# Kernel tuning notes

Measured on AMD Instinct MI355X. Metric: run time of the kernel, lower is better.

Reference implementation:

```python
import jax, jax.numpy as jnp
from jax import lax
import numpy as np

B, H, W = 8, 1024, 1024
NUM_POINTS = 10
THRESHOLD_RATIO = 0.5
K_PEAKS = 512  # cap on peak candidates fed to greedy NMS


def setup_inputs() -> dict:
    key = jax.random.key(0)
    ks = jax.random.split(key, 8)
    return {
        "rgb_image": jax.random.uniform(ks[0], (B, 3, H, W), jnp.float32),
        "depth_image": jax.random.uniform(ks[1], (B, 1, H, W), jnp.float32),
        "conv1_w": jax.random.normal(ks[2], (32, 12, 3, 3), jnp.float32) * 0.1,
        "conv1_b": jax.random.normal(ks[3], (32,), jnp.float32) * 0.1,
        "bn_gamma": jnp.ones((32,), jnp.float32),
        "bn_beta": jnp.zeros((32,), jnp.float32),
        "bn_mean": jax.random.normal(ks[4], (32,), jnp.float32) * 0.1,
        "bn_var": jax.random.uniform(ks[5], (32,), jnp.float32) + 0.5,
        "conv2_w": jax.random.normal(ks[6], (1, 32, 1, 1), jnp.float32) * 0.1,
        "conv2_b": jnp.zeros((1,), jnp.float32),
    }


def dwt2(x):
    # Haar DWT exactly as in the torch module (row split then column split)
    x01 = x[..., 0::2, :] * 0.5
    x02 = x[..., 1::2, :] * 0.5
    LL = x01[..., 0::2] + x02[..., 0::2]
    LH = x01[..., 0::2] - x02[..., 0::2]
    HL = x01[..., 1::2] + x02[..., 1::2]
    HH = x01[..., 1::2] - x02[..., 1::2]
    return LL, LH, HL, HH


def conv2d(x, w, b=None, pad=0, groups=1):
    y = lax.conv_general_dilated(x, w, (1, 1), [(pad, pad), (pad, pad)],
                                 dimension_numbers=("NCHW", "OIHW", "NCHW"),
                                 feature_group_count=groups)
    if b is not None:
        y = y + b[None, :, None, None]
    return y


def gaussian_smooth(x, k=5, sigma=1.0):
    ax = jnp.arange(-(k // 2), k // 2 + 1, dtype=jnp.float32)
    xx, yy = jnp.meshgrid(ax, ax, indexing="ij")
    ker = jnp.exp(-(xx ** 2 + yy ** 2) / (2.0 * sigma ** 2))
    ker = ker / ker.sum()
    C = x.shape[1]
    wk = jnp.tile(ker[None, None], (C, 1, 1, 1))  # depthwise
    return conv2d(x, wk, pad=k // 2, groups=C)


def find_points(s):
    """Greedy spatial-NMS peak picking on a single (h,w) saliency map.
    Returns (NUM_POINTS, 2) normalized (x, y) coords."""
    h, w = s.shape
    min_dist = float(max(max(h, w) // 20, 20))
    flat = s.reshape(-1)
    mp = lax.reduce_window(s, -jnp.inf, lax.max, (3, 3), (1, 1), [(1, 1), (1, 1)])
    peak_flat = ((s == mp) & (s > 0)).reshape(-1)
    peak_scores = jnp.where(peak_flat, flat, -jnp.inf)
    top_vals, top_idx = lax.top_k(peak_scores, K_PEAKS)  # sorted desc = torch argsort
    valid = top_vals > -jnp.inf
    px = (top_idx % w).astype(jnp.float32)
    py = (top_idx // w).astype(jnp.float32)
    pc = jnp.stack([px, py], axis=-1)                     # (K,2)
    dist = jnp.sqrt(((pc[:, None, :] - pc[None, :, :]) ** 2).sum(-1))  # (K,K)
    ar = jnp.arange(K_PEAKS)

    def body(i, st):
        avail, sel, cnt = st
        take = avail[i] & valid[i] & (cnt < NUM_POINTS)
        sel = sel.at[i].set(take)
        suppress = (dist[i] < min_dist) & (ar > i)  # nearby[:i+1]=False in torch
        avail = jnp.where(take, avail & (~suppress), avail)
        return avail, sel, cnt + take.astype(jnp.int32)

    _, sel, n_chosen = lax.fori_loop(
        0, K_PEAKS, body,
        (jnp.ones(K_PEAKS, bool), jnp.zeros(K_PEAKS, bool), jnp.int32(0)))

    # compact chosen peak indices (in descending-score order) into first slots
    pos = jnp.cumsum(sel.astype(jnp.int32)) - 1
    scatter_pos = jnp.where(sel, pos, NUM_POINTS)  # out-of-range -> dropped
    buf = jnp.zeros(NUM_POINTS, jnp.int32).at[scatter_pos].set(top_idx, mode="drop")
    # fallback: top saliency excluding all peaks (matches torch fill-up branch)
    fb_scores = jnp.where(peak_flat, -jnp.inf, flat)
    _, fb_idx = lax.top_k(fb_scores, NUM_POINTS)
    slot = jnp.arange(NUM_POINTS)
    fb = fb_idx[jnp.clip(slot - n_chosen, 0, NUM_POINTS - 1)]
    sel_idx = jnp.where(slot < n_chosen, buf, fb)
    cx = (sel_idx % w).astype(jnp.float32) / w
    cy = (sel_idx // w).astype(jnp.float32) / h
    return jnp.stack([cx, cy], axis=-1)


def boxes_from_mask(masks):
    binm = masks[:, 0] > THRESHOLD_RATIO  # (B,H,W)
    Hh, Ww = binm.shape[1], binm.shape[2]
    rows = binm.any(axis=2)
    cols = binm.any(axis=1)
    ri = jnp.arange(Hh)
    ci = jnp.arange(Ww)
    rmin = jnp.min(jnp.where(rows, ri[None, :], Hh), axis=1)
    rmax = jnp.max(jnp.where(rows, ri[None, :], -1), axis=1)
    cmin = jnp.min(jnp.where(cols, ci[None, :], Ww), axis=1)
    cmax = jnp.max(jnp.where(cols, ci[None, :], -1), axis=1)
    has = rows.any(axis=1)
    boxes = jnp.stack([cmin, rmin, cmax, rmax], axis=-1).astype(jnp.float32)
    default = jnp.array([0.0, 0.0, Ww - 1.0, Hh - 1.0], jnp.float32)
    return jnp.where(has[:, None], boxes, default[None, :])


def reference(rgb_image, depth_image, conv1_w, conv1_b, bn_gamma, bn_beta,
              bn_mean, bn_var, conv2_w, conv2_b):
    rgb_gray = rgb_image.mean(axis=1, keepdims=True)
    rLL, rLH, rHL, rHH = dwt2(rgb_gray)
    dLL, dLH, dHL, dHH = dwt2(depth_image)
    E_rgb = jnp.sqrt(rLH ** 2 + rHL ** 2 + rHH ** 2 + 1e-8)
    E_depth = jnp.sqrt(dLH ** 2 + dHL ** 2 + dHH ** 2 + 1e-8)
    E_rgb_s = gaussian_smooth(E_rgb)
    E_depth_s = gaussian_smooth(E_depth)
    freq = jnp.concatenate(
        [rLL, rLH, rHL, rHH, dLL, dLH, dHL, dHH, E_rgb, E_depth, E_rgb_s, E_depth_s],
        axis=1)  # (B,12,H/2,W/2)
    x = conv2d(freq, conv1_w, conv1_b, pad=1)
    inv = lax.rsqrt(bn_var + 1e-5)
    x = bn_gamma[None, :, None, None] * (x - bn_mean[None, :, None, None]) * inv[None, :, None, None] + bn_beta[None, :, None, None]
    x = jax.nn.gelu(x)
    sal = jax.nn.sigmoid(conv2d(x, conv2_w, conv2_b))  # (B,1,H/2,W/2)
    masks = jax.image.resize(sal, (sal.shape[0], 1, H, W), method="bilinear")
    coords = jax.vmap(find_points)(sal[:, 0])          # (B,N,2)
    labels = jnp.ones((sal.shape[0], NUM_POINTS), jnp.int32)
    boxes = boxes_from_mask(masks)                     # (B,4)
    return coords, labels, boxes, masks
```

## Files before the change

kernel.cpp:

```cpp
#include <hip/hip_runtime.h>
#include <math.h>


#define CHW 262144
#define FULLHW 1048576
#define NB1 64
#define NB2 32

typedef __attribute__((ext_vector_type(8))) short bf16x8;
typedef __attribute__((ext_vector_type(4))) float f32x4;

static __device__ __forceinline__ unsigned short f2bf(float x) {
  unsigned u = __float_as_uint(x);
  u += 0x7FFFu + ((u >> 16) & 1u);
  return (unsigned short)(u >> 16);
}
static __device__ __forceinline__ float bf2f(unsigned short h) {
  return __uint_as_float(((unsigned)h) << 16);
}

static constexpr size_t OFF_SAL   = 0;
static constexpr size_t OFF_THR   = 8388608;
static constexpr size_t OFF_CNT   = OFF_THR + 256;
static constexpr size_t OFF_CAND  = OFF_CNT + 256;
static constexpr size_t OFF_PART  = OFF_CAND + 131072;
static constexpr size_t OFF_APACK = OFF_PART + 32768;
static constexpr size_t OFF_EP    = OFF_APACK + 20480;
static constexpr size_t OFF_PKM   = OFF_EP + 512;
static constexpr size_t OFF_DYN   = OFF_PKM + 2097152;

static constexpr int KDY[10] = {-1,-1,-1, 0,0,0, 1,1,1, 0};
static constexpr int KDX[10] = {-1, 0, 1,-1,0,1,-1,0,1, 0};

__global__ void k_init(unsigned* __restrict__ cnt,
                       const float* __restrict__ w1, const float* __restrict__ b1,
                       const float* __restrict__ gam, const float* __restrict__ bet,
                       const float* __restrict__ mean, const float* __restrict__ var,
                       const float* __restrict__ w2, const float* __restrict__ b2,
                       unsigned short* __restrict__ apack, float* __restrict__ ep) {
  int i = blockIdx.x * 256 + threadIdx.x;
  if (i < 16) cnt[i] = 0;
  if (i < 10240) {
    int frag = i >> 9, lane = (i >> 3) & 63, e = i & 7;
    int hh = frag & 1, mtks = frag >> 1;
    int mt = mtks / 5, ks = mtks % 5;
    int co = mt * 16 + (lane & 15);
    int k = ((lane >> 4) << 3) + e;
    int c = k & 15, shift = ks * 2 + (k >> 4);
    float val = (shift < 9 && c < 12) ? w1[co * 108 + c * 9 + shift] : 0.0f;
    unsigned short hb = f2bf(val);
    apack[i] = hh ? f2bf(val - bf2f(hb)) : hb;
  }
  int j = i - 10240;
  if (j >= 0 && j < 97) {
    if (j < 32) {
      ep[j] = gam[j] * rsqrtf(var[j] + 1e-5f);
    } else if (j < 64) {
      int c = j - 32;
      float sc = gam[c] * rsqrtf(var[c] + 1e-5f);
      ep[j] = (b1[c] - mean[c]) * sc + bet[c];
    } else if (j < 96) {
      ep[j] = w2[j - 64];
    } else {
      ep[j] = b2[0];
    }
  }
}

__global__ __launch_bounds__(256) void k_freq(const float* __restrict__ rgb,
                                              const float* __restrict__ dep,
                                              unsigned short* __restrict__ freq2,
                                              float* __restrict__ ebuf, int b0) {
  int t = blockIdx.x * 256 + threadIdx.x;
  int bi = blockIdx.y;
  int b = b0 + bi;
  int xp = t & 255, y = t >> 8;
  const float* base = rgb + (size_t)b * 3 * FULLHW + (size_t)(2 * y) * 1024 + 4 * xp;
  float4 R0 = *(const float4*)(base);
  float4 R1 = *(const float4*)(base + 1024);
  float4 G0 = *(const float4*)(base + FULLHW);
  float4 G1 = *(const float4*)(base + FULLHW + 1024);
  float4 Bl0 = *(const float4*)(base + 2 * FULLHW);
  float4 Bl1 = *(const float4*)(base + 2 * FULLHW + 1024);
  const float* dbase = dep + (size_t)b * FULLHW + (size_t)(2 * y) * 1024 + 4 * xp;
  float4 D0 = *(const float4*)(dbase);
  float4 D1 = *(const float4*)(dbase + 1024);

  float gt[4], gb[4], dt[4], db_[4];
  gt[0] = (R0.x + G0.x + Bl0.x) / 3.0f; gt[1] = (R0.y + G0.y + Bl0.y) / 3.0f;
  gt[2] = (R0.z + G0.z + Bl0.z) / 3.0f; gt[3] = (R0.w + G0.w + Bl0.w) / 3.0f;
  gb[0] = (R1.x + G1.x + Bl1.x) / 3.0f; gb[1] = (R1.y + G1.y + Bl1.y) / 3.0f;
  gb[2] = (R1.z + G1.z + Bl1.z) / 3.0f; gb[3] = (R1.w + G1.w + Bl1.w) / 3.0f;
  dt[0] = D0.x; dt[1] = D0.y; dt[2] = D0.z; dt[3] = D0.w;
  db_[0] = D1.x; db_[1] = D1.y; db_[2] = D1.z; db_[3] = D1.w;

  unsigned short hs[2][16], ls[2][16];
  float er[2], ed[2];
  #pragma unroll
  for (int j = 0; j < 2; ++j) {
    float a = gt[2 * j] * 0.5f, bb = gb[2 * j] * 0.5f;
    float c = gt[2 * j + 1] * 0.5f, d = gb[2 * j + 1] * 0.5f;
    float v[10];
    v[0] = a + bb; v[1] = a - bb; v[2] = c + d; v[3] = c - d;
    float da = dt[2 * j] * 0.5f, db2 = db_[2 * j] * 0.5f;
    float dc = dt[2 * j + 1] * 0.5f, dd = db_[2 * j + 1] * 0.5f;
    v[4] = da + db2; v[5] = da - db2; v[6] = dc + dd; v[7] = dc - dd;
    v[8] = sqrtf(v[1] * v[1] + v[2] * v[2] + v[3] * v[3] + 1e-8f);
    v[9] = sqrtf(v[5] * v[5] + v[6] * v[6] + v[7] * v[7] + 1e-8f);
    er[j] = v[8]; ed[j] = v[9];
    #pragma unroll
    for (int cc = 0; cc < 10; ++cc) {
      unsigned short hb = f2bf(v[cc]);
      hs[j][cc] = hb;
      ls[j][cc] = f2bf(v[cc] - bf2f(hb));
    }
    #pragma unroll
    for (int cc = 10; cc < 16; ++cc) { hs[j][cc] = 0; ls[j][cc] = 0; }
  }
  unsigned short* dst = freq2 + (size_t)bi * CHW * 32 + (size_t)(y * 512 + 2 * xp) * 32;
  uint4* d4 = (uint4*)dst;
  d4[0] = ((const uint4*)hs[0])[0]; d4[1] = ((const uint4*)hs[0])[1];
  d4[2] = ((const uint4*)ls[0])[0]; d4[3] = ((const uint4*)ls[0])[1];
  d4[4] = ((const uint4*)hs[1])[0]; d4[5] = ((const uint4*)hs[1])[1];
  d4[6] = ((const uint4*)ls[1])[0]; d4[7] = ((const uint4*)ls[1])[1];
  float* eb = ebuf + (size_t)bi * 2 * CHW + (size_t)y * 512 + 2 * xp;
  *(float2*)(eb) = make_float2(er[0], er[1]);
  *(float2*)(eb + CHW) = make_float2(ed[0], ed[1]);
}

__constant__ float GW[25] = {
  0.00296901f, 0.01330621f, 0.02193824f, 0.01330621f, 0.00296901f,
  0.01330621f, 0.05963435f, 0.09832035f, 0.05963435f, 0.01330621f,
  0.02193824f, 0.09832035f, 0.16210276f, 0.09832035f, 0.02193824f,
  0.01330621f, 0.05963435f, 0.09832035f, 0.05963435f, 0.01330621f,
  0.00296901f, 0.01330621f, 0.02193824f, 0.01330621f, 0.00296901f};

__global__ __launch_bounds__(256) void k_smooth(const float* __restrict__ ebuf,
                                                unsigned short* __restrict__ freq2) {
  int t = blockIdx.x * 256 + threadIdx.x;
  int bi = blockIdx.y;
  int x = t & 511, y = t >> 9;
  const float* eb = ebuf + (size_t)bi * 2 * CHW;
  float accv[2];
  #pragma unroll
  for (int ch = 0; ch < 2; ++ch) {
    const float* fin = eb + ch * CHW;
    float acc = 0.0f;
    #pragma unroll
    for (int i = 0; i < 5; ++i) {
      int yy = y + i - 2;
      if (yy < 0 || yy > 511) continue;
      #pragma unroll
      for (int j = 0; j < 5; ++j) {
        int xx = x + j - 2;
        if (xx < 0 || xx > 511) continue;
        acc += GW[i * 5 + j] * fin[yy * 512 + xx];
      }
    }
    accv[ch] = acc;
  }
  unsigned short* px = freq2 + (size_t)bi * CHW * 32 + (size_t)t * 32;
  unsigned short h0 = f2bf(accv[0]), h1 = f2bf(accv[1]);
  unsigned short l0 = f2bf(accv[0] - bf2f(h0)), l1 = f2bf(accv[1] - bf2f(h1));
  *(unsigned*)(px + 10) = (unsigned)h0 | ((unsigned)h1 << 16);
  *(unsigned*)(px + 26) = (unsigned)l0 | ((unsigned)l1 << 16);
}

__global__ __launch_bounds__(256) void k_conv(const unsigned short* __restrict__ freq2,
    const unsigned short* __restrict__ apack, const float* __restrict__ ep,
    float* __restrict__ sal, int b0) {
  int tid = threadIdx.x;
  int l = tid & 63, wv = tid >> 6;
  int y = blockIdx.y;
  int xw = blockIdx.x * 128 + wv * 32;
  int bi = blockIdx.z;
  const unsigned short* fb = freq2 + (size_t)bi * CHW * 32;

  int ln = l & 15, lg = l >> 4;
  int sl = lg >> 1;
  int c0 = (lg & 1) << 3;

  float sc[8], sh[8], w2v[8];
  #pragma unroll
  for (int mt = 0; mt < 2; ++mt)
    #pragma unroll
    for (int r = 0; r < 4; ++r) {
      int co = mt * 16 + lg * 4 + r;
      sc[mt * 4 + r]  = ep[co];
      sh[mt * 4 + r]  = ep[32 + co];
      w2v[mt * 4 + r] = ep[64 + co];
    }
  float b2v = ep[96];

  f32x4 acc[2][2] = {};

  #pragma unroll
  for (int ks = 0; ks < 5; ++ks) {
    int dy = sl ? KDY[ks * 2 + 1] : KDY[ks * 2];
    int dx = sl ? KDX[ks * 2 + 1] : KDX[ks * 2];
    int yy = y + dy;
    bool yok = (unsigned)yy < 512u;
    bf16x8 Ah[2], Al[2];
    #pragma unroll
    for (int mt = 0; mt < 2; ++mt) {
      const unsigned short* ab = apack + ((size_t)((mt * 5 + ks) * 2) * 64 + l) * 8;
      Ah[mt] = *(const bf16x8*)(ab);
      Al[mt] = *(const bf16x8*)(ab + 512);
    }
    #pragma unroll
    for (int nt = 0; nt < 2; ++nt) {
      int xx = xw + nt * 16 + ln + dx;
      bf16x8 Bh = {}, Bl = {};
      if (yok && (unsigned)xx < 512u) {
        const unsigned short* pb = fb + (size_t)(yy * 512 + xx) * 32 + c0;
        Bh = *(const bf16x8*)(pb);
        Bl = *(const bf16x8*)(pb + 16);
      }
      #pragma unroll
      for (int mt = 0; mt < 2; ++mt) {
        acc[mt][nt] = __builtin_amdgcn_mfma_f32_16x16x32_bf16(Ah[mt], Bh, acc[mt][nt], 0, 0, 0);
        acc[mt][nt] = __builtin_amdgcn_mfma_f32_16x16x32_bf16(Al[mt], Bh, acc[mt][nt], 0, 0, 0);
        acc[mt][nt] = __builtin_amdgcn_mfma_f32_16x16x32_bf16(Ah[mt], Bl, acc[mt][nt], 0, 0, 0);
      }
    }
  }

  #pragma unroll
  for (int nt = 0; nt < 2; ++nt) {
    float s2 = 0.0f;
    #pragma unroll
    for (int mt = 0; mt < 2; ++mt)
      #pragma unroll
      for (int r = 0; r < 4; ++r) {
        float t = acc[mt][nt][r] * sc[mt * 4 + r] + sh[mt * 4 + r];
        float t2 = t * t;
        float z = t * (1.5957691216057308f + 0.07135481283247183f * t2);
        float g = t / (1.0f + __expf(-z));
        s2 += g * w2v[mt * 4 + r];
      }
    s2 += __shfl_xor(s2, 16);
    s2 += __shfl_xor(s2, 32);
    s2 += b2v;
    float res = 1.0f / (1.0f + __expf(-s2));
    if (lg == 0)
      sal[(size_t)(b0 + bi) * CHW + (size_t)y * 512 + xw + nt * 16 + ln] = res;
  }
}

__global__ __launch_bounds__(256) void k_resize(const float* __restrict__ sal,
                                                float* __restrict__ masks,
                                                int* __restrict__ part) {
  int b = blockIdx.y;
  int blk = blockIdx.x;
  int t = threadIdx.x;
  const float* sp = sal + (size_t)b * CHW;
  float* mp = masks + (size_t)b * FULLHW;
  int mnX = 0x7FFFFFFF, mxX = -1, mnY = 0x7FFFFFFF, mxY = -1;
  int c0 = 4 * t;
  #pragma unroll
  for (int r = 0; r < 4; ++r) {
    int Y = blk * 4 + r;
    int y0 = (Y - 1) >> 1;
    float wy = (Y & 1) ? 0.25f : 0.75f;
    int y0c = y0 < 0 ? 0 : y0, y1c = (y0 + 1 > 511) ? 511 : y0 + 1;
    const float* r0 = sp + y0c * 512;
    const float* r1 = sp + y1c * 512;
    float o[4];
    #pragma unroll
    for (int j = 0; j < 4; ++j) {
      int X = c0 + j;
      int x0 = (X - 1) >> 1;
      float wx = (X & 1) ? 0.25f : 0.75f;
      int x0c = x0 < 0 ? 0 : x0, x1c = (x0 + 1 > 511) ? 511 : x0 + 1;
      float v00 = r0[x0c], v01 = r0[x1c], v10 = r1[x0c], v11 = r1[x1c];
      o[j] = (1.0f - wy) * ((1.0f - wx) * v00 + wx * v01)
           + wy * ((1.0f - wx) * v10 + wx * v11);
      if (o[j] > 0.5f) {
        mnX = min(mnX, X); mxX = max(mxX, X);
        mnY = min(mnY, Y); mxY = max(mxY, Y);
      }
    }
    *(float4*)(mp + (size_t)Y * 1024 + c0) = make_float4(o[0], o[1], o[2], o[3]);
  }
  __shared__ int s0[256], s1[256], s2[256], s3[256];
  s0[t] = mnX; s1[t] = mxX; s2[t] = mnY; s3[t] = mxY;
  __syncthreads();
  for (int off = 128; off > 0; off >>= 1) {
    if (t < off) {
      s0[t] = min(s0[t], s0[t + off]); s1[t] = max(s1[t], s1[t + off]);
      s2[t] = min(s2[t], s2[t + off]); s3[t] = max(s3[t], s3[t + off]);
    }
    __syncthreads();
  }
  if (t == 0) {
    int* pp = part + (b * 256 + blk) * 4;
    pp[0] = s0[0]; pp[1] = s1[0]; pp[2] = s2[0]; pp[3] = s3[0];
  }
}

__global__ __launch_bounds__(256) void k_boxreduce(const int* __restrict__ part,
                                                   float* __restrict__ out) {
  int b = blockIdx.x, t = threadIdx.x;
  const int* pp = part + (b * 256 + t) * 4;
  __shared__ int s0[256], s1[256], s2[256], s3[256];
  s0[t] = pp[0]; s1[t] = pp[1]; s2[t] = pp[2]; s3[t] = pp[3];
  __syncthreads();
  for (int off = 128; off > 0; off >>= 1) {
    if (t < off) {
      s0[t] = min(s0[t], s0[t + off]); s1[t] = max(s1[t], s1[t + off]);
      s2[t] = min(s2[t], s2[t + off]); s3[t] = max(s3[t], s3[t + off]);
    }
    __syncthreads();
  }
  if (t == 0) {
    float x0, y0, x1, y1;
    if (s3[0] < 0) { x0 = 0.0f; y0 = 0.0f; x1 = 1023.0f; y1 = 1023.0f; }
    else { x0 = (float)s0[0]; y0 = (float)s2[0]; x1 = (float)s1[0]; y1 = (float)s3[0]; }
    out[240 + b * 4 + 0] = x0;
    out[240 + b * 4 + 1] = y0;
    out[240 + b * 4 + 2] = x1;
    out[240 + b * 4 + 3] = y1;
  }
}

__device__ inline bool is_peak(const float* __restrict__ sp, int x, int y, float& sv) {
  float s = sp[y * 512 + x];
  sv = s;
  if (!(s > 0.0f)) return false;
  int x0 = (x > 0) ? x - 1 : x, x1 = (x < 511) ? x + 1 : x;
  int y0 = (y > 0) ? y - 1 : y, y1 = (y < 511) ? y + 1 : y;
  for (int yy = y0; yy <= y1; ++yy)
    for (int xx = x0; xx <= x1; ++xx)
      if (sp[yy * 512 + xx] > s) return false;
  return true;
}

__global__ __launch_bounds__(256) void k_hist1(const float* __restrict__ sal,
                                               unsigned* __restrict__ h1p,
                                               unsigned char* __restrict__ pkm) {
  __shared__ unsigned sH[4096];
  int b = blockIdx.y, tid = threadIdx.x;
  for (int i = tid; i < 4096; i += 256) sH[i] = 0;
  __syncthreads();
  const float* sp = sal + (size_t)b * CHW;
  int base = blockIdx.x * 4096;
  for (int it = 0; it < 16; ++it) {
    int p = base + it * 256 + tid;
    int x = p & 511, y = p >> 9;
    float s;
    bool pk = is_peak(sp, x, y, s);
    pkm[(size_t)b * CHW + p] = pk ? 1 : 0;
    unsigned bin = (__float_as_uint(s) >> 21) & 2047;
    atomicAdd(&sH[(pk ? 0 : 2048) + bin], 1u);
  }
  __syncthreads();
  unsigned* dst = h1p + ((size_t)b * NB1 + blockIdx.x) * 4096;
  for (int i = tid; i < 4096; i += 256) dst[i] = sH[i];
}

__global__ __launch_bounds__(256) void k_scan(const unsigned* __restrict__ hp,
                                              int* __restrict__ thr, int level,
                                              int np) {
  int c = blockIdx.x, b = blockIdx.y, t = threadIdx.x;
  __shared__ unsigned sBins[2048];
  __shared__ unsigned sS[256];
  __shared__ int sT;
  unsigned bv[8] = {0, 0, 0, 0, 0, 0, 0, 0};
  for (int p = 0; p < np; ++p) {
    const unsigned* q = hp + ((size_t)(b * np + p)) * 4096 + c * 2048 + t * 8;
    uint4 a = *(const uint4*)(q);
    uint4 d = *(const uint4*)(q + 4);
    bv[0] += a.x; bv[1] += a.y; bv[2] += a.z; bv[3] += a.w;
    bv[4] += d.x; bv[5] += d.y; bv[6] += d.z; bv[7] += d.w;
  }
  unsigned part = 0;
  #pragma unroll
  for (int r = 0; r < 8; ++r) {
    sBins[t * 8 + r] = bv[r];
    part += bv[r];
  }
  sS[t] = part;
  __syncthreads();
  for (int off = 1; off < 256; off <<= 1) {
    unsigned add = (t + off < 256) ? sS[t + off] : 0;
    __syncthreads();
    sS[t] += add;
    __syncthreads();
  }
  int K = (c == 0) ? 512 : 10;
  int* tb = thr + (c * 8 + b) * 4;
  if (level == 1) { K -= tb[1]; if (K < 1) K = 1; }
  if (t == 0) sT = -1;
  __syncthreads();
  if (sS[t] >= (unsigned)K && (t == 255 || sS[t + 1] < (unsigned)K)) sT = t;
  __syncthreads();
  if (t == 0) {
    int T = 0;
    unsigned run = 0;
    if (sT >= 0) {
      int ts = sT;
      run = (ts < 255) ? sS[ts + 1] : 0;
      for (int r = 7; r >= 0; --r) {
        unsigned v = sBins[ts * 8 + r];
        run += v;
        if (run >= (unsigned)K) { T = ts * 8 + r; run -= v; break; }
      }
    } else {
      T = 0;
      run = sS[0] - sBins[0];
    }
    if (level == 0) { tb[0] = T; tb[1] = (int)run; }
    else           { tb[2] = (tb[0] << 11) | T; }
  }
}

__global__ __launch_bounds__(256) void k_hist2(const float* __restrict__ sal,
                                               const unsigned char* __restrict__ pkm,
                                               const int* __restrict__ thr,
                                               unsigned* __restrict__ h2p) {
  __shared__ unsigned sH[4096];
  int b = blockIdx.y, tid = threadIdx.x;
  for (int i = tid; i < 4096; i += 256) sH[i] = 0;
  __syncthreads();
  int t0 = thr[(0 * 8 + b) * 4];
  int t1 = thr[(1 * 8 + b) * 4];
  const float* sp = sal + (size_t)b * CHW;
  const unsigned char* pp = pkm + (size_t)b * CHW;
  int base = blockIdx.x * 8192;
  for (int it = 0; it < 8; ++it) {
    int p = base + it * 1024 + tid * 4;
    float4 s4 = *(const float4*)(sp + p);
    unsigned pk4 = *(const unsigned*)(pp + p);
    float sv[4] = {s4.x, s4.y, s4.z, s4.w};
    #pragma unroll
    for (int j = 0; j < 4; ++j) {
      bool pk = ((pk4 >> (8 * j)) & 255u) != 0;
      unsigned bits = __float_as_uint(sv[j]);
      int tt = pk ? t0 : t1;
      if ((int)(bits >> 21) == tt)
        atomicAdd(&sH[(pk ? 0 : 2048) + ((bits >> 10) & 2047)], 1u);
    }
  }
  __syncthreads();
  unsigned* dst = h2p + ((size_t)b * NB2 + blockIdx.x) * 4096;
  for (int i = tid; i < 4096; i += 256) dst[i] = sH[i];
}

__global__ __launch_bounds__(256) void k_compact(const float* __restrict__ sal,
                                                 const unsigned char* __restrict__ pkm,
                                                 const int* __restrict__ thr,
                                                 unsigned* __restrict__ cnt,
                                                 unsigned long long* __restrict__ cand) {
  int b = blockIdx.y;
  int p = blockIdx.x * 256 + threadIdx.x;
  const float* sp = sal + (size_t)b * CHW;
  bool pk = pkm[(size_t)b * CHW + p] != 0;
  float s = sp[p];
  int c = pk ? 0 : 1;
  unsigned bits = __float_as_uint(s);
  unsigned q = (unsigned)thr[(c * 8 + b) * 4 + 2];
  if ((bits >> 10) >= q) {
    unsigned pos = atomicAdd(&cnt[c * 8 + b], 1u);
    if (pos < 1024)
      cand[((size_t)(c * 8 + b) << 10) + pos] =
          ((unsigned long long)bits << 32) | (unsigned)(~p);
  }
}

__device__ inline void bitonic1024_desc(unsigned long long* sKey) {
  int t = threadIdx.x;
  for (unsigned k = 2; k <= 1024; k <<= 1) {
    for (unsigned j = k >> 1; j > 0; j >>= 1) {
      __syncthreads();
      #pragma unroll
      for (int e = 0; e < 2; ++e) {
        unsigned i = (unsigned)t + (unsigned)e * 512u;
        unsigned l = i ^ j;
        if (l > i) {
          unsigned long long a = sKey[i], bb = sKey[l];
          if (((i & k) == 0) ? (a < bb) : (a > bb)) { sKey[i] = bb; sKey[l] = a; }
        }
      }
    }
  }
  __syncthreads();
}

__global__ __launch_bounds__(512) void k_nms(const unsigned long long* __restrict__ cand,
                                             const unsigned* __restrict__ cnt,
                                             float* __restrict__ out) {
  __shared__ unsigned long long sKey[1024];
  __shared__ unsigned sIdx[512];
  __shared__ int sAvail[512];
  __shared__ int sSel[16];
  int b = blockIdx.x, t = threadIdx.x;
  if (t < 10) out[160 + b * 10 + t] = 1.0f;
  int Cp = (int)cnt[b]; if (Cp > 1024) Cp = 1024;
  const unsigned long long* cp = cand + ((size_t)b << 10);
  sKey[t] = (t < Cp) ? cp[t] : 0ULL;
  sKey[t + 512] = (t + 512 < Cp) ? cp[t + 512] : 0ULL;
  bitonic1024_desc(sKey);
  sIdx[t] = (unsigned)(~sKey[t]);
  int ncand = (Cp < 512) ? Cp : 512;
  sAvail[t] = (t < ncand) ? 1 : 0;
  __syncthreads();
  int nsel = 0;
  for (int i = 0; i < 512 && nsel < 10; ++i) {
    if (sAvail[i] != 0) {
      unsigned pi = sIdx[i];
      int xi = (int)(pi & 511), yi = (int)(pi >> 9);
      if (t > i && sAvail[t]) {
        int dx = (int)(sIdx[t] & 511) - xi;
        int dy = (int)(sIdx[t] >> 9) - yi;
        if (dx * dx + dy * dy < 625) sAvail[t] = 0;
      }
      if (t == 0) sSel[nsel] = (int)pi;
      ++nsel;
      __syncthreads();
    }
  }
  __syncthreads();
  int Cf = (int)cnt[8 + b]; if (Cf > 1024) Cf = 1024;
  const unsigned long long* cf = cand + ((size_t)(8 + b) << 10);
  sKey[t] = (t < Cf) ? cf[t] : 0ULL;
  sKey[t + 512] = (t + 512 < Cf) ? cf[t + 512] : 0ULL;
  bitonic1024_desc(sKey);
  if (t < 10) {
    int fi;
    if (t < nsel) fi = sSel[t];
    else { int r = t - nsel; if (r > 9) r = 9; fi = (int)((unsigned)(~sKey[r])); }
    out[((size_t)b * 10 + t) * 2 + 0] = (float)(fi & 511) * (1.0f / 512.0f);
    out[((size_t)b * 10 + t) * 2 + 1] = (float)(fi >> 9) * (1.0f / 512.0f);
  }
}

extern "C" void kernel_launch(void* const* d_in, const int* in_sizes, int n_in,
                              void* d_out, int out_size, void* d_ws, size_t ws_size,
                              hipStream_t stream) {
  const float* rgb  = (const float*)d_in[0];
  const float* dep  = (const float*)d_in[1];
  const float* w1   = (const float*)d_in[2];
  const float* b1   = (const float*)d_in[3];
  const float* gam  = (const float*)d_in[4];
  const float* bet  = (const float*)d_in[5];
  const float* bmn  = (const float*)d_in[6];
  const float* bvr  = (const float*)d_in[7];
  const float* w2   = (const float*)d_in[8];
  const float* b2   = (const float*)d_in[9];
  float* out = (float*)d_out;
  char* ws = (char*)d_ws;

  float* sal = (float*)(ws + OFF_SAL);
  int* thr = (int*)(ws + OFF_THR);
  unsigned* cnt = (unsigned*)(ws + OFF_CNT);
  unsigned long long* cand = (unsigned long long*)(ws + OFF_CAND);
  int* part = (int*)(ws + OFF_PART);
  unsigned short* apack = (unsigned short*)(ws + OFF_APACK);
  float* ep = (float*)(ws + OFF_EP);
  unsigned char* pkm = (unsigned char*)(ws + OFF_PKM);

  size_t perE = (size_t)2 * CHW * 4;
  size_t perF = (size_t)CHW * 64;
  long long avail = (long long)ws_size - (long long)OFF_DYN;
  int nb = 1;
  if (avail >= (long long)(perE + perF)) {
    long long m = avail / (long long)(perE + perF);
    nb = (m > 8) ? 8 : (int)m;
  }
  float* ebuf = (float*)(ws + OFF_DYN);
  unsigned short* freq2 = (unsigned short*)(ws + OFF_DYN + perE * (size_t)nb);
  unsigned* h1p = (unsigned*)(ws + OFF_DYN);
  unsigned* h2p = (unsigned*)(ws + OFF_DYN + (size_t)8 * NB1 * 4096 * 4);

  k_init<<<256, 256, 0, stream>>>(cnt, w1, b1, gam, bet, bmn, bvr, w2, b2,
                                  apack, ep);

  for (int b0 = 0; b0 < 8; b0 += nb) {
    int nbc = (8 - b0 < nb) ? (8 - b0) : nb;
    k_freq<<<dim3(512, nbc), 256, 0, stream>>>(rgb, dep, freq2, ebuf, b0);
    k_smooth<<<dim3(1024, nbc), 256, 0, stream>>>(ebuf, freq2);
    k_conv<<<dim3(4, 512, nbc), 256, 0, stream>>>(freq2, apack, ep, sal, b0);
  }

  k_resize<<<dim3(256, 8), 256, 0, stream>>>(sal, out + 272, part);
  k_boxreduce<<<8, 256, 0, stream>>>(part, out);
  k_hist1<<<dim3(NB1, 8), 256, 0, stream>>>(sal, h1p, pkm);
  k_scan<<<dim3(2, 8), 256, 0, stream>>>(h1p, thr, 0, NB1);
  k_hist2<<<dim3(NB2, 8), 256, 0, stream>>>(sal, pkm, thr, h2p);
  k_scan<<<dim3(2, 8), 256, 0, stream>>>(h2p, thr, 1, NB2);
  k_compact<<<dim3(1024, 8), 256, 0, stream>>>(sal, pkm, thr, cnt, cand);
  k_nms<<<8, 512, 0, stream>>>(cand, cnt, out);
}
```

Measured before the change: 611.8 us.

## Pad freq buffer with zero halo and use 32x32 MFMA conv

The intermediate frequency buffer gets a one-pixel zero border so the 3x3 conv no longer needs boundary checks. The conv kernel switches from 16x16x32 to 32x32x16 bf16 MFMA, with one fragment per kernel tap, and the packed weights and epilogue layouts are rebuilt to match. The peak detection in hist1 and the candidate compaction are vectorized to handle four pixels per thread with float4 loads. The aim is less branching and indexing overhead and fewer MFMA issues in the conv stage, plus fewer scalar loads in the post-processing passes. In exchange, the padded buffer needs a separate border-zeroing kernel and a slightly larger workspace.

```diff
diff --git a/kernel.cpp b/kernel.cpp
--- a/kernel.cpp
+++ b/kernel.cpp
@@ -6,9 +6,11 @@
 #define FULLHW 1048576
 #define NB1 64
 #define NB2 32
+#define PROW 514
+#define PREC (514*514)
 
 typedef __attribute__((ext_vector_type(8))) short bf16x8;
-typedef __attribute__((ext_vector_type(4))) float f32x4;
+typedef __attribute__((ext_vector_type(16))) float f32x16;
 
 static __device__ __forceinline__ unsigned short f2bf(float x) {
   unsigned u = __float_as_uint(x);
@@ -29,8 +31,8 @@
 static constexpr size_t OFF_PKM   = OFF_EP + 512;
 static constexpr size_t OFF_DYN   = OFF_PKM + 2097152;
 
-static constexpr int KDY[10] = {-1,-1,-1, 0,0,0, 1,1,1, 0};
-static constexpr int KDX[10] = {-1, 0, 1,-1,0,1,-1,0,1, 0};
+static constexpr int SDY[9] = {-1,-1,-1, 0,0,0, 1,1,1};
+static constexpr int SDX[9] = {-1, 0, 1,-1,0,1,-1,0,1};
 
 __global__ void k_init(unsigned* __restrict__ cnt,
                        const float* __restrict__ w1, const float* __restrict__ b1,
@@ -40,31 +42,40 @@
                        unsigned short* __restrict__ apack, float* __restrict__ ep) {
   int i = blockIdx.x * 256 + threadIdx.x;
   if (i < 16) cnt[i] = 0;
-  if (i < 10240) {
-    int frag = i >> 9, lane = (i >> 3) & 63, e = i & 7;
-    int hh = frag & 1, mtks = frag >> 1;
-    int mt = mtks / 5, ks = mtks % 5;
-    int co = mt * 16 + (lane & 15);
-    int k = ((lane >> 4) << 3) + e;
-    int c = k & 15, shift = ks * 2 + (k >> 4);
-    float val = (shift < 9 && c < 12) ? w1[co * 108 + c * 9 + shift] : 0.0f;
+  if (i < 9216) {
+    int e = i & 7, lane = (i >> 3) & 63, frag = i >> 9;
+    int s = frag >> 1, hh = frag & 1;
+    int co = lane & 31;
+    int c = ((lane >> 5) << 3) + e;
+    float val = (c < 12) ? w1[co * 108 + c * 9 + s] : 0.0f;
     unsigned short hb = f2bf(val);
     apack[i] = hh ? f2bf(val - bf2f(hb)) : hb;
   }
-  int j = i - 10240;
-  if (j >= 0 && j < 97) {
-    if (j < 32) {
-      ep[j] = gam[j] * rsqrtf(var[j] + 1e-5f);
-    } else if (j < 64) {
-      int c = j - 32;
-      float sc = gam[c] * rsqrtf(var[c] + 1e-5f);
-      ep[j] = (b1[c] - mean[c]) * sc + bet[c];
-    } else if (j < 96) {
-      ep[j] = w2[j - 64];
-    } else {
-      ep[j] = b2[0];
-    }
-  }
+  if (i < 96) {
+    int t = i >> 5, rem = i & 31, kg = rem >> 4, reg = rem & 15;
+    int co = (reg & 3) + 8 * (reg >> 2) + 4 * kg;
+    float sc = gam[co] * rsqrtf(var[co] + 1e-5f);
+    float v = (t == 0) ? sc
+            : (t == 1) ? (b1[co] - mean[co]) * sc + bet[co]
+                       : w2[co];
+    ep[i] = v;
+  } else if (i == 96) {
+    ep[96] = b2[0];
+  }
+}
+
+__global__ __launch_bounds__(256) void k_zero(unsigned short* __restrict__ freq2) {
+  int i = blockIdx.x * 256 + threadIdx.x;
+  int bi = blockIdx.y;
+  if (i >= 8208) return;
+  int rec = i >> 2, q = i & 3;
+  int row, col;
+  if (rec < 514)       { row = 0;   col = rec; }
+  else if (rec < 1028) { row = 513; col = rec - 514; }
+  else if (rec < 1540) { row = rec - 1028 + 1; col = 0; }
+  else                 { row = rec - 1540 + 1; col = 513; }
+  uint4* p = (uint4*)(freq2 + ((size_t)bi * PREC + (size_t)row * PROW + col) * 32) + q;
+  *p = make_uint4(0u, 0u, 0u, 0u);
 }
 
 __global__ __launch_bounds__(256) void k_freq(const float* __restrict__ rgb,
@@ -117,7 +128,8 @@
     #pragma unroll
     for (int cc = 10; cc < 16; ++cc) { hs[j][cc] = 0; ls[j][cc] = 0; }
   }
-  unsigned short* dst = freq2 + (size_t)bi * CHW * 32 + (size_t)(y * 512 + 2 * xp) * 32;
+  unsigned short* dst = freq2 +
+      ((size_t)bi * PREC + (size_t)(y + 1) * PROW + (2 * xp + 1)) * 32;
   uint4* d4 = (uint4*)dst;
   d4[0] = ((const uint4*)hs[0])[0]; d4[1] = ((const uint4*)hs[0])[1];
   d4[2] = ((const uint4*)ls[0])[0]; d4[3] = ((const uint4*)ls[0])[1];
@@ -159,7 +171,8 @@
     }
     accv[ch] = acc;
   }
-  unsigned short* px = freq2 + (size_t)bi * CHW * 32 + (size_t)t * 32;
+  unsigned short* px = freq2 +
+      ((size_t)bi * PREC + (size_t)(y + 1) * PROW + (x + 1)) * 32;
   unsigned short h0 = f2bf(accv[0]), h1 = f2bf(accv[1]);
   unsigned short l0 = f2bf(accv[0] - bf2f(h0)), l1 = f2bf(accv[1] - bf2f(h1));
   *(unsigned*)(px + 10) = (unsigned)h0 | ((unsigned)h1 << 16);
@@ -174,77 +187,41 @@
   int y = blockIdx.y;
   int xw = blockIdx.x * 128 + wv * 32;
   int bi = blockIdx.z;
-  const unsigned short* fb = freq2 + (size_t)bi * CHW * 32;
-
-  int ln = l & 15, lg = l >> 4;
-  int sl = lg >> 1;
-  int c0 = (lg & 1) << 3;
-
-  float sc[8], sh[8], w2v[8];
-  #pragma unroll
-  for (int mt = 0; mt < 2; ++mt)
-    #pragma unroll
-    for (int r = 0; r < 4; ++r) {
-      int co = mt * 16 + lg * 4 + r;
-      sc[mt * 4 + r]  = ep[co];
-      sh[mt * 4 + r]  = ep[32 + co];
-      w2v[mt * 4 + r] = ep[64 + co];
-    }
-  float b2v = ep[96];
-
-  f32x4 acc[2][2] = {};
-
-  #pragma unroll
-  for (int ks = 0; ks < 5; ++ks) {
-    int dy = sl ? KDY[ks * 2 + 1] : KDY[ks * 2];
-    int dx = sl ? KDX[ks * 2 + 1] : KDX[ks * 2];
-    int yy = y + dy;
-    bool yok = (unsigned)yy < 512u;
-    bf16x8 Ah[2], Al[2];
-    #pragma unroll
-    for (int mt = 0; mt < 2; ++mt) {
-      const unsigned short* ab = apack + ((size_t)((mt * 5 + ks) * 2) * 64 + l) * 8;
-      Ah[mt] = *(const bf16x8*)(ab);
-      Al[mt] = *(const bf16x8*)(ab + 512);
-    }
-    #pragma unroll
-    for (int nt = 0; nt < 2; ++nt) {
-      int xx = xw + nt * 16 + ln + dx;
-      bf16x8 Bh = {}, Bl = {};
-      if (yok && (unsigned)xx < 512u) {
-        const unsigned short* pb = fb + (size_t)(yy * 512 + xx) * 32 + c0;
-        Bh = *(const bf16x8*)(pb);
-        Bl = *(const bf16x8*)(pb + 16);
-      }
-      #pragma unroll
-      for (int mt = 0; mt < 2; ++mt) {
-        acc[mt][nt] = __builtin_amdgcn_mfma_f32_16x16x32_bf16(Ah[mt], Bh, acc[mt][nt], 0, 0, 0);
-        acc[mt][nt] = __builtin_amdgcn_mfma_f32_16x16x32_bf16(Al[mt], Bh, acc[mt][nt], 0, 0, 0);
-        acc[mt][nt] = __builtin_amdgcn_mfma_f32_16x16x32_bf16(Ah[mt], Bl, acc[mt][nt], 0, 0, 0);
-      }
-    }
-  }
-
-  #pragma unroll
-  for (int nt = 0; nt < 2; ++nt) {
-    float s2 = 0.0f;
-    #pragma unroll
-    for (int mt = 0; mt < 2; ++mt)
-      #pragma unroll
-      for (int r = 0; r < 4; ++r) {
-        float t = acc[mt][nt][r] * sc[mt * 4 + r] + sh[mt * 4 + r];
-        float t2 = t * t;
-        float z = t * (1.5957691216057308f + 0.07135481283247183f * t2);
-        float g = t / (1.0f + __expf(-z));
-        s2 += g * w2v[mt * 4 + r];
-      }
-    s2 += __shfl_xor(s2, 16);
-    s2 += __shfl_xor(s2, 32);
-    s2 += b2v;
-    float res = 1.0f / (1.0f + __expf(-s2));
-    if (lg == 0)
-      sal[(size_t)(b0 + bi) * CHW + (size_t)y * 512 + xw + nt * 16 + ln] = res;
-  }
+  int n = l & 31, kg = l >> 5;
+
+  const unsigned short* fb = freq2 + (size_t)bi * PREC * 32;
+  const unsigned short* pb0 = fb + ((size_t)(y + 1) * PROW + (xw + n + 1)) * 32 + kg * 8;
+  const unsigned short* ab = apack + l * 8;
+
+  f32x16 acc = {};
+  #pragma unroll
+  for (int s = 0; s < 9; ++s) {
+    const int doff = (SDY[s] * PROW + SDX[s]) * 32;
+    const unsigned short* pb = pb0 + doff;
+    bf16x8 Bh = *(const bf16x8*)(pb);
+    bf16x8 Bl = *(const bf16x8*)(pb + 16);
+    bf16x8 Ah = *(const bf16x8*)(ab + s * 1024);
+    bf16x8 Al = *(const bf16x8*)(ab + s * 1024 + 512);
+    acc = __builtin_amdgcn_mfma_f32_32x32x16_bf16(Ah, Bh, acc, 0, 0, 0);
+    acc = __builtin_amdgcn_mfma_f32_32x32x16_bf16(Al, Bh, acc, 0, 0, 0);
+    acc = __builtin_amdgcn_mfma_f32_32x32x16_bf16(Ah, Bl, acc, 0, 0, 0);
+  }
+
+  const float* e0 = ep + kg * 16;
+  const float* e1 = ep + 32 + kg * 16;
+  const float* e2 = ep + 64 + kg * 16;
+  float s2 = 0.0f;
+  #pragma unroll
+  for (int r = 0; r < 16; ++r) {
+    float t = acc[r] * e0[r] + e1[r];
+    float z = t * (1.5957691216057308f + 0.07135481283247183f * (t * t));
+    s2 += (t / (1.0f + __expf(-z))) * e2[r];
+  }
+  s2 += __shfl_xor(s2, 32);
+  s2 += ep[96];
+  float res = 1.0f / (1.0f + __expf(-s2));
+  if (l < 32)
+    sal[(size_t)(b0 + bi) * CHW + (size_t)y * 512 + xw + n] = res;
 }
 
 __global__ __launch_bounds__(256) void k_resize(const float* __restrict__ sal,
@@ -323,18 +300,6 @@
   }
 }
 
-__device__ inline bool is_peak(const float* __restrict__ sp, int x, int y, float& sv) {
-  float s = sp[y * 512 + x];
-  sv = s;
-  if (!(s > 0.0f)) return false;
-  int x0 = (x > 0) ? x - 1 : x, x1 = (x < 511) ? x + 1 : x;
-  int y0 = (y > 0) ? y - 1 : y, y1 = (y < 511) ? y + 1 : y;
-  for (int yy = y0; yy <= y1; ++yy)
-    for (int xx = x0; xx <= x1; ++xx)
-      if (sp[yy * 512 + xx] > s) return false;
-  return true;
-}
-
 __global__ __launch_bounds__(256) void k_hist1(const float* __restrict__ sal,
                                                unsigned* __restrict__ h1p,
                                                unsigned char* __restrict__ pkm) {
@@ -344,14 +309,39 @@
   __syncthreads();
   const float* sp = sal + (size_t)b * CHW;
   int base = blockIdx.x * 4096;
-  for (int it = 0; it < 16; ++it) {
-    int p = base + it * 256 + tid;
-    int x = p & 511, y = p >> 9;
-    float s;
-    bool pk = is_peak(sp, x, y, s);
-    pkm[(size_t)b * CHW + p] = pk ? 1 : 0;
-    unsigned bin = (__float_as_uint(s) >> 21) & 2047;
-    atomicAdd(&sH[(pk ? 0 : 2048) + bin], 1u);
+  for (int it = 0; it < 4; ++it) {
+    int p = base + it * 1024 + tid * 4;
+    int x0 = p & 511, y = p >> 9;
+    int ym = (y > 0) ? y - 1 : 0, yp = (y < 511) ? y + 1 : 511;
+    const float* r0 = sp + ym * 512;
+    const float* r1 = sp + y * 512;
+    const float* r2 = sp + yp * 512;
+    float4 m0 = *(const float4*)(r0 + x0);
+    float4 m1 = *(const float4*)(r1 + x0);
+    float4 m2 = *(const float4*)(r2 + x0);
+    float l0 = x0 ? r0[x0 - 1] : m0.x;
+    float l1 = x0 ? r1[x0 - 1] : m1.x;
+    float l2 = x0 ? r2[x0 - 1] : m2.x;
+    float q0 = (x0 < 508) ? r0[x0 + 4] : m0.w;
+    float q1 = (x0 < 508) ? r1[x0 + 4] : m1.w;
+    float q2 = (x0 < 508) ? r2[x0 + 4] : m2.w;
+    float a0[6] = {l0, m0.x, m0.y, m0.z, m0.w, q0};
+    float a1[6] = {l1, m1.x, m1.y, m1.z, m1.w, q1};
+    float a2[6] = {l2, m2.x, m2.y, m2.z, m2.w, q2};
+    unsigned pw = 0;
+    #pragma unroll
+    for (int j = 0; j < 4; ++j) {
+      float r0m = fmaxf(fmaxf(a0[j], a0[j + 1]), a0[j + 2]);
+      float r1m = fmaxf(fmaxf(a1[j], a1[j + 1]), a1[j + 2]);
+      float r2m = fmaxf(fmaxf(a2[j], a2[j + 1]), a2[j + 2]);
+      float cmax = fmaxf(fmaxf(r0m, r1m), r2m);
+      float sv = a1[j + 1];
+      bool pk = (sv > 0.0f) && (sv >= cmax);
+      pw |= (pk ? 1u : 0u) << (8 * j);
+      unsigned bin = (__float_as_uint(sv) >> 21) & 2047;
+      atomicAdd(&sH[(pk ? 0 : 2048) + bin], 1u);
+    }
+    *(unsigned*)(pkm + (size_t)b * CHW + p) = pw;
   }
   __syncthreads();
   unsigned* dst = h1p + ((size_t)b * NB1 + blockIdx.x) * 4096;
@@ -452,18 +442,25 @@
                                                  unsigned* __restrict__ cnt,
                                                  unsigned long long* __restrict__ cand) {
   int b = blockIdx.y;
-  int p = blockIdx.x * 256 + threadIdx.x;
+  int p = (blockIdx.x * 256 + threadIdx.x) * 4;
   const float* sp = sal + (size_t)b * CHW;
-  bool pk = pkm[(size_t)b * CHW + p] != 0;
-  float s = sp[p];
-  int c = pk ? 0 : 1;
-  unsigned bits = __float_as_uint(s);
-  unsigned q = (unsigned)thr[(c * 8 + b) * 4 + 2];
-  if ((bits >> 10) >= q) {
-    unsigned pos = atomicAdd(&cnt[c * 8 + b], 1u);
-    if (pos < 1024)
-      cand[((size_t)(c * 8 + b) << 10) + pos] =
-          ((unsigned long long)bits << 32) | (unsigned)(~p);
+  float4 s4 = *(const float4*)(sp + p);
+  unsigned pk4 = *(const unsigned*)(pkm + (size_t)b * CHW + p);
+  unsigned q0 = (unsigned)thr[(0 * 8 + b) * 4 + 2];
+  unsigned q1 = (unsigned)thr[(1 * 8 + b) * 4 + 2];
+  float sv[4] = {s4.x, s4.y, s4.z, s4.w};
+  #pragma unroll
+  for (int j = 0; j < 4; ++j) {
+    bool pk = ((pk4 >> (8 * j)) & 255u) != 0;
+    unsigned bits = __float_as_uint(sv[j]);
+    unsigned q = pk ? q0 : q1;
+    int c = pk ? 0 : 1;
+    if ((bits >> 10) >= q) {
+      unsigned pos = atomicAdd(&cnt[c * 8 + b], 1u);
+      if (pos < 1024)
+        cand[((size_t)(c * 8 + b) << 10) + pos] =
+            ((unsigned long long)bits << 32) | (unsigned)(~(p + j));
+    }
   }
 }
 
@@ -560,7 +557,7 @@
   unsigned char* pkm = (unsigned char*)(ws + OFF_PKM);
 
   size_t perE = (size_t)2 * CHW * 4;
-  size_t perF = (size_t)CHW * 64;
+  size_t perF = (size_t)PREC * 64;
   long long avail = (long long)ws_size - (long long)OFF_DYN;
   int nb = 1;
   if (avail >= (long long)(perE + perF)) {
@@ -572,8 +569,9 @@
   unsigned* h1p = (unsigned*)(ws + OFF_DYN);
   unsigned* h2p = (unsigned*)(ws + OFF_DYN + (size_t)8 * NB1 * 4096 * 4);
 
-  k_init<<<256, 256, 0, stream>>>(cnt, w1, b1, gam, bet, bmn, bvr, w2, b2,
-                                  apack, ep);
+  k_init<<<40, 256, 0, stream>>>(cnt, w1, b1, gam, bet, bmn, bvr, w2, b2,
+                                 apack, ep);
+  k_zero<<<dim3(33, nb), 256, 0, stream>>>(freq2);
 
   for (int b0 = 0; b0 < 8; b0 += nb) {
     int nbc = (8 - b0 < nb) ? (8 - b0) : nb;
@@ -588,6 +586,6 @@
   k_scan<<<dim3(2, 8), 256, 0, stream>>>(h1p, thr, 0, NB1);
   k_hist2<<<dim3(NB2, 8), 256, 0, stream>>>(sal, pkm, thr, h2p);
   k_scan<<<dim3(2, 8), 256, 0, stream>>>(h2p, thr, 1, NB2);
-  k_compact<<<dim3(1024, 8), 256, 0, stream>>>(sal, pkm, thr, cnt, cand);
+  k_compact<<<dim3(256, 8), 256, 0, stream>>>(sal, pkm, thr, cnt, cand);
   k_nms<<<8, 512, 0, stream>>>(cand, cnt, out);
 }
```

Measured after the change: 581.7 us. 4.9% less time.
